# Kernel optimization log

Measured on AMD Instinct MI355X. Metric: run time of the kernel, lower is better.

## Reference

```python
import jax, jax.numpy as jnp
import numpy as np

B, D_IN, H, D_OUT, E = 16384, 512, 1024, 512, 4


def setup_inputs() -> dict:
    key = jax.random.key(0)
    ks = jax.random.split(key, 8)
    x = jax.random.normal(ks[0], (B, D_IN), dtype=jnp.float32)
    command = jax.random.randint(ks[1], (B,), 0, E, dtype=jnp.int64)
    # Per-branch Encoder params: Linear(D_IN->H), Linear(H->H), Linear(H->D_OUT)
    s = 0.02
    W1 = jax.random.normal(ks[2], (E, D_IN, H), dtype=jnp.float32) * s
    b1 = jnp.zeros((E, H), dtype=jnp.float32)
    W2 = jax.random.normal(ks[3], (E, H, H), dtype=jnp.float32) * s
    b2 = jnp.zeros((E, H), dtype=jnp.float32)
    W3 = jax.random.normal(ks[4], (E, H, D_OUT), dtype=jnp.float32) * s
    b3 = jnp.zeros((E, D_OUT), dtype=jnp.float32)
    return {"x": x, "command": command, "W1": W1, "b1": b1,
            "W2": W2, "b2": b2, "W3": W3, "b3": b3}


def reference(x, command, W1, b1, W2, b2, W3, b3):
    # Evaluate all branches as batched GEMMs, then select per-sample branch.
    # Mathematically identical to per-sample dispatch in the torch module.
    h = jax.nn.relu(jnp.einsum('bi,eih->beh', x, W1) + b1)        # [B,E,H]
    h = jax.nn.relu(jnp.einsum('beh,ehk->bek', h, W2) + b2)       # [B,E,H]
    y = jnp.tanh(jnp.einsum('bek,eko->beo', h, W3) + b3)          # [B,E,D_OUT]
    # select branch output per sample according to command
    idx = command.astype(jnp.int32)[:, None, None]                # [B,1,1]
    out = jnp.take_along_axis(y, idx, axis=1)[:, 0, :]            # [B,D_OUT]
    return out
```

## Files before the change

kernel.cpp:

```cpp
#include <hip/hip_runtime.h>


#define B_N   16384
#define DIN   512
#define HID   1024
#define DOUT  512
#define MAXTILES 136

typedef __attribute__((ext_vector_type(8))) short bf16x8;
typedef __attribute__((ext_vector_type(4))) float f32x4;
typedef __attribute__((address_space(3))) unsigned int lds_u32;
typedef const __attribute__((address_space(1))) unsigned int glb_u32;

__device__ __forceinline__ void gll16(const void* g, void* l) {
    __builtin_amdgcn_global_load_lds((glb_u32*)g, (lds_u32*)l, 16, 0, 0);
}

__device__ __forceinline__ unsigned short f2bf(float f) {
    unsigned int u = __float_as_uint(f);
    u += 0x7FFFu + ((u >> 16) & 1u);
    return (unsigned short)(u >> 16);
}

__device__ __forceinline__ float fast_tanh(float x) {
    x = fminf(fmaxf(x, -9.0f), 9.0f);
    float t = __builtin_amdgcn_exp2f(x * 2.8853900817779268f);
    return (t - 1.0f) * __builtin_amdgcn_rcpf(t + 1.0f);
}

__global__ void plan_all_k(const int* __restrict__ cmd, int* __restrict__ ctrl,
                           int* __restrict__ tileExpert, int* __restrict__ tileBase) {
    __shared__ int h[4];
    int tid = threadIdx.x;
    if (tid < 4) h[tid] = 0;
    __syncthreads();
    int c0 = 0, c1 = 0, c2 = 0, c3 = 0;
    for (int i = tid; i < B_N; i += 256) {
        int e = cmd[i] & 3;
        c0 += (e == 0); c1 += (e == 1); c2 += (e == 2); c3 += (e == 3);
    }
    atomicAdd(&h[0], c0); atomicAdd(&h[1], c1);
    atomicAdd(&h[2], c2); atomicAdd(&h[3], c3);
    __syncthreads();
    if (tid == 0) {
        int P = 0, nt = 0;
        for (int e = 0; e < 4; ++e) {
            ctrl[e] = h[e];
            ctrl[4 + e] = 0;
            ctrl[8 + e] = P;
            int tiles = (h[e] + 127) >> 7;
            for (int t = 0; t < tiles; ++t) {
                tileExpert[nt] = e;
                tileBase[nt] = P + t * 128;
                ++nt;
            }
            P += tiles * 128;
        }
        ctrl[12] = P;
        ctrl[13] = nt;
    }
}

__global__ void scatter_k(const int* __restrict__ cmd, int* __restrict__ ctrl,
                          int* __restrict__ perm) {
    int i = blockIdx.x * 256 + threadIdx.x;
    int e = cmd[i] & 3;
    int lane = threadIdx.x & 63;
#pragma unroll
    for (int ee = 0; ee < 4; ++ee) {
        unsigned long long mask = __ballot(e == ee);
        if (e == ee) {
            int leader = __ffsll((unsigned long long)mask) - 1;
            int rank = __popcll(mask & ((1ull << lane) - 1ull));
            int wbase = 0;
            if (lane == leader)
                wbase = atomicAdd(&ctrl[4 + ee], __popcll(mask));
            wbase = __builtin_amdgcn_readfirstlane(wbase);
            perm[ctrl[8 + ee] + wbase + rank] = i;
        }
    }
}

__global__ __launch_bounds__(256) void prep_data_k(
    const float* __restrict__ W1, const float* __restrict__ W2,
    const float* __restrict__ W3, unsigned short* __restrict__ Wt1,
    unsigned short* __restrict__ Wt2, unsigned short* __restrict__ Wt3,
    const float* __restrict__ x, unsigned short* __restrict__ xp,
    int* __restrict__ perm, const int* __restrict__ ctrl)
{
    int b = blockIdx.x;
    if (b < 8192) {
        int e = b >> 11, r = b & 2047;
        const float* W; unsigned short* Wt; int KD, ND, kt, nt;
        if (r < 512)       { W = W1; Wt = Wt1; KD = 512;  ND = 1024; kt = r & 15;           nt = r >> 4; }
        else if (r < 1536) { W = W2; Wt = Wt2; KD = 1024; ND = 1024; kt = (r - 512) & 31;   nt = (r - 512) >> 5; }
        else               { W = W3; Wt = Wt3; KD = 1024; ND = 512;  kt = (r - 1536) & 31;  nt = (r - 1536) >> 5; }
        __shared__ float t[32][33];
        size_t base = (size_t)e * KD * ND;
        int k0 = kt * 32, n0 = nt * 32;
        int tx = threadIdx.x & 31, ty = threadIdx.x >> 5;
#pragma unroll
        for (int s = 0; s < 4; ++s)
            t[ty + s * 8][tx] = W[base + (size_t)(k0 + ty + s * 8) * ND + n0 + tx];
        __syncthreads();
#pragma unroll
        for (int s = 0; s < 4; ++s)
            Wt[base + (size_t)(n0 + ty + s * 8) * KD + k0 + tx] = f2bf(t[tx][ty + s * 8]);
    } else {
        int g = b - 8192;
        int p = g * 4 + (int)(threadIdx.x >> 6);
        if (p >= ctrl[12]) return;
        int lane = threadIdx.x & 63;
        int e = (p >= ctrl[9]) + (p >= ctrl[10]) + (p >= ctrl[11]);
        int segBase = ctrl[8 + e];
        int src;
        if (p < segBase + ctrl[e]) {
            src = perm[p];
        } else {
            src = perm[segBase];
            if (lane == 0) perm[p] = src;
        }
        const float* xr = x + (size_t)src * DIN + lane * 8;
        float4 a = *(const float4*)xr;
        float4 c = *(const float4*)(xr + 4);
        uint4 o;
        o.x = (unsigned)f2bf(a.x) | ((unsigned)f2bf(a.y) << 16);
        o.y = (unsigned)f2bf(a.z) | ((unsigned)f2bf(a.w) << 16);
        o.z = (unsigned)f2bf(c.x) | ((unsigned)f2bf(c.y) << 16);
        o.w = (unsigned)f2bf(c.z) | ((unsigned)f2bf(c.w) << 16);
        *(uint4*)(xp + (size_t)p * DIN + lane * 8) = o;
    }
}

template<int K, int N, int ACT, bool SCATTER_OUT>
__global__ __launch_bounds__(256) void gemm_k(
    const unsigned short* __restrict__ A, const unsigned short* __restrict__ Bt,
    const float* __restrict__ bias, void* __restrict__ Outp,
    const int* __restrict__ ctrl, const int* __restrict__ tileExpert,
    const int* __restrict__ tileBase, const int* __restrict__ perm)
{
    if ((int)blockIdx.x >= ctrl[13]) return;
    const int e = tileExpert[blockIdx.x];
    const int rowBase = tileBase[blockIdx.x];
    const int n0 = blockIdx.y * 128;

    __shared__ unsigned short Als[128 * 64];
    __shared__ unsigned short Bls[128 * 64];

    const int tid = threadIdx.x;
    const int lane = tid & 63;
    const int w = tid >> 6;
    const int wm = w >> 1, wn = w & 1;
    const int lr = lane & 15, lh = lane >> 4;

    f32x4 acc[4][4] = {};

    const int tr = tid >> 3;
    const int tc = tid & 7;
    const int cs = (tc ^ (tr & 7)) * 8;
    const unsigned short* As = A + (size_t)(rowBase + tr) * K + cs;
    const unsigned short* Bs = Bt + ((size_t)e * N + n0 + tr) * K + cs;
    const int ldst = tr * 64 + tc * 8;

    constexpr int NK = K / 64;
    for (int kq = 0; kq < NK; ++kq) {
        const int k0 = kq * 64;
        __syncthreads();
#pragma unroll
        for (int j = 0; j < 4; ++j) {
            gll16(As + (size_t)(j * 32) * K + k0, &Als[j * 2048 + ldst]);
            gll16(Bs + (size_t)(j * 32) * K + k0, &Bls[j * 2048 + ldst]);
        }
        __syncthreads();
#pragma unroll
        for (int kk = 0; kk < 2; ++kk) {
            const int ksl = ((kk * 4 + lh) ^ (lr & 7)) * 8;
            bf16x8 afr[4], bfr[4];
#pragma unroll
            for (int mi = 0; mi < 4; ++mi)
                afr[mi] = *(const bf16x8*)&Als[(wm * 64 + mi * 16 + lr) * 64 + ksl];
#pragma unroll
            for (int ni = 0; ni < 4; ++ni)
                bfr[ni] = *(const bf16x8*)&Bls[(wn * 64 + ni * 16 + lr) * 64 + ksl];
#pragma unroll
            for (int mi = 0; mi < 4; ++mi)
#pragma unroll
                for (int ni = 0; ni < 4; ++ni)
                    acc[mi][ni] = __builtin_amdgcn_mfma_f32_16x16x32_bf16(
                        afr[mi], bfr[ni], acc[mi][ni], 0, 0, 0);
        }
    }

    float bv[4];
    int colv[4];
#pragma unroll
    for (int ni = 0; ni < 4; ++ni) {
        colv[ni] = n0 + wn * 64 + ni * 16 + lr;
        bv[ni] = bias[e * N + colv[ni]];
    }
#pragma unroll
    for (int mi = 0; mi < 4; ++mi) {
#pragma unroll
        for (int r = 0; r < 4; ++r) {
            int rowL = wm * 64 + mi * 16 + lh * 4 + r;
            int gRow = rowBase + rowL;
            int orow = SCATTER_OUT ? perm[gRow] : gRow;
#pragma unroll
            for (int ni = 0; ni < 4; ++ni) {
                float v = acc[mi][ni][r] + bv[ni];
                if (ACT == 0) v = fmaxf(v, 0.0f);
                else          v = fast_tanh(v);
                if (SCATTER_OUT)
                    ((float*)Outp)[(size_t)orow * N + colv[ni]] = v;
                else
                    ((unsigned short*)Outp)[(size_t)orow * N + colv[ni]] = f2bf(v);
            }
        }
    }
}

extern "C" void kernel_launch(void* const* d_in, const int* in_sizes, int n_in,
                              void* d_out, int out_size, void* d_ws, size_t ws_size,
                              hipStream_t stream) {
    const float* x  = (const float*)d_in[0];
    const int*   cmd= (const int*)d_in[1];
    const float* W1 = (const float*)d_in[2];
    const float* b1 = (const float*)d_in[3];
    const float* W2 = (const float*)d_in[4];
    const float* b2 = (const float*)d_in[5];
    const float* W3 = (const float*)d_in[6];
    const float* b3 = (const float*)d_in[7];
    float* out = (float*)d_out;

    char* w = (char*)d_ws;
    int* ctrl       = (int*)w;
    int* tileExpert = ctrl + 64;
    int* tileBase   = ctrl + 224;
    int* perm       = ctrl + 512;
    unsigned short* Wt1 = (unsigned short*)(w + 131072);
    unsigned short* Wt2 = (unsigned short*)(w + 131072 + 4194304);
    unsigned short* Wt3 = (unsigned short*)(w + 131072 + 12582912);
    unsigned short* h1  = (unsigned short*)(w + 131072 + 16777216);
    unsigned short* h2  = h1 + (size_t)16896 * HID;
    unsigned short* xp  = h2;

    plan_all_k<<<1, 256, 0, stream>>>(cmd, ctrl, tileExpert, tileBase);
    scatter_k<<<B_N / 256, 256, 0, stream>>>(cmd, ctrl, perm);
    prep_data_k<<<8192 + 4224, 256, 0, stream>>>(W1, W2, W3, Wt1, Wt2, Wt3,
                                                 x, xp, perm, ctrl);

    gemm_k<DIN, HID, 0, false><<<dim3(MAXTILES, 8), 256, 0, stream>>>(
        xp, Wt1, b1, h1, ctrl, tileExpert, tileBase, perm);
    gemm_k<HID, HID, 0, false><<<dim3(MAXTILES, 8), 256, 0, stream>>>(
        h1, Wt2, b2, h2, ctrl, tileExpert, tileBase, perm);
    gemm_k<HID, DOUT, 1, true><<<dim3(MAXTILES, 4), 256, 0, stream>>>(
        h2, Wt3, b3, out, ctrl, tileExpert, tileBase, perm);
}
```

Measured before the change: 167.9 us.

## Overlap W2/W3 transpose-convert with first GEMM via extra blocks

The prep kernel now transposes and converts only W1 plus the gathered x. The W2 and W3 fp32-to-bf16 transposes move into extra blocks appended to the first GEMM's grid, so they run alongside the layer-1 matrix work instead of before it. This hides the weight conversion bandwidth behind compute. In exchange the GEMM launch has a much larger grid and the shared memory is reused as transpose scratch.

```diff
diff --git a/kernel.cpp b/kernel.cpp
--- a/kernel.cpp
+++ b/kernel.cpp
@@ -81,33 +81,28 @@
     }
 }
 
-__global__ __launch_bounds__(256) void prep_data_k(
-    const float* __restrict__ W1, const float* __restrict__ W2,
-    const float* __restrict__ W3, unsigned short* __restrict__ Wt1,
-    unsigned short* __restrict__ Wt2, unsigned short* __restrict__ Wt3,
+__global__ __launch_bounds__(256) void prep1_k(
+    const float* __restrict__ W1, unsigned short* __restrict__ Wt1,
     const float* __restrict__ x, unsigned short* __restrict__ xp,
     int* __restrict__ perm, const int* __restrict__ ctrl)
 {
     int b = blockIdx.x;
-    if (b < 8192) {
-        int e = b >> 11, r = b & 2047;
-        const float* W; unsigned short* Wt; int KD, ND, kt, nt;
-        if (r < 512)       { W = W1; Wt = Wt1; KD = 512;  ND = 1024; kt = r & 15;           nt = r >> 4; }
-        else if (r < 1536) { W = W2; Wt = Wt2; KD = 1024; ND = 1024; kt = (r - 512) & 31;   nt = (r - 512) >> 5; }
-        else               { W = W3; Wt = Wt3; KD = 1024; ND = 512;  kt = (r - 1536) & 31;  nt = (r - 1536) >> 5; }
+    if (b < 2048) {
+        int e = b >> 9, r = b & 511;
+        int kt = r & 15, nt = r >> 4;
         __shared__ float t[32][33];
-        size_t base = (size_t)e * KD * ND;
+        size_t base = (size_t)e * DIN * HID;
         int k0 = kt * 32, n0 = nt * 32;
         int tx = threadIdx.x & 31, ty = threadIdx.x >> 5;
 #pragma unroll
         for (int s = 0; s < 4; ++s)
-            t[ty + s * 8][tx] = W[base + (size_t)(k0 + ty + s * 8) * ND + n0 + tx];
-        __syncthreads();
-#pragma unroll
-        for (int s = 0; s < 4; ++s)
-            Wt[base + (size_t)(n0 + ty + s * 8) * KD + k0 + tx] = f2bf(t[tx][ty + s * 8]);
+            t[ty + s * 8][tx] = W1[base + (size_t)(k0 + ty + s * 8) * HID + n0 + tx];
+        __syncthreads();
+#pragma unroll
+        for (int s = 0; s < 4; ++s)
+            Wt1[base + (size_t)(n0 + ty + s * 8) * DIN + k0 + tx] = f2bf(t[tx][ty + s * 8]);
     } else {
-        int g = b - 8192;
+        int g = b - 2048;
         int p = g * 4 + (int)(threadIdx.x >> 6);
         if (p >= ctrl[12]) return;
         int lane = threadIdx.x & 63;
@@ -132,20 +127,43 @@
     }
 }
 
-template<int K, int N, int ACT, bool SCATTER_OUT>
+template<int K, int N, int ACT, bool SCATTER_OUT, bool FUSE_TW>
 __global__ __launch_bounds__(256) void gemm_k(
     const unsigned short* __restrict__ A, const unsigned short* __restrict__ Bt,
     const float* __restrict__ bias, void* __restrict__ Outp,
     const int* __restrict__ ctrl, const int* __restrict__ tileExpert,
-    const int* __restrict__ tileBase, const int* __restrict__ perm)
+    const int* __restrict__ tileBase, const int* __restrict__ perm,
+    const float* __restrict__ W2, const float* __restrict__ W3,
+    unsigned short* __restrict__ Wt2, unsigned short* __restrict__ Wt3)
 {
+    __shared__ unsigned short Als[128 * 64];
+    __shared__ unsigned short Bls[128 * 64];
+
+    if (FUSE_TW && (int)blockIdx.x >= MAXTILES) {
+        int T = ((int)blockIdx.x - MAXTILES) + 768 * (int)blockIdx.y;
+        const float* W; unsigned short* Wt; int KD, ND, kt, nt, e;
+        if (T < 4096) { W = W2; Wt = Wt2; KD = HID; ND = HID;
+                        e = T >> 10; int r = T & 1023; kt = r & 31; nt = r >> 5; }
+        else { int T2 = T - 4096; W = W3; Wt = Wt3; KD = HID; ND = DOUT;
+               e = T2 >> 9; int r = T2 & 511; kt = r & 31; nt = r >> 5; }
+        float (*t)[33] = (float(*)[33])Als;
+        size_t base = (size_t)e * KD * ND;
+        int k0 = kt * 32, n0 = nt * 32;
+        int tx = threadIdx.x & 31, ty = threadIdx.x >> 5;
+#pragma unroll
+        for (int s = 0; s < 4; ++s)
+            t[ty + s * 8][tx] = W[base + (size_t)(k0 + ty + s * 8) * ND + n0 + tx];
+        __syncthreads();
+#pragma unroll
+        for (int s = 0; s < 4; ++s)
+            Wt[base + (size_t)(n0 + ty + s * 8) * KD + k0 + tx] = f2bf(t[tx][ty + s * 8]);
+        return;
+    }
+
     if ((int)blockIdx.x >= ctrl[13]) return;
     const int e = tileExpert[blockIdx.x];
     const int rowBase = tileBase[blockIdx.x];
     const int n0 = blockIdx.y * 128;
-
-    __shared__ unsigned short Als[128 * 64];
-    __shared__ unsigned short Bls[128 * 64];
 
     const int tid = threadIdx.x;
     const int lane = tid & 63;
@@ -246,13 +264,14 @@
 
     plan_all_k<<<1, 256, 0, stream>>>(cmd, ctrl, tileExpert, tileBase);
     scatter_k<<<B_N / 256, 256, 0, stream>>>(cmd, ctrl, perm);
-    prep_data_k<<<8192 + 4224, 256, 0, stream>>>(W1, W2, W3, Wt1, Wt2, Wt3,
-                                                 x, xp, perm, ctrl);
-
-    gemm_k<DIN, HID, 0, false><<<dim3(MAXTILES, 8), 256, 0, stream>>>(
-        xp, Wt1, b1, h1, ctrl, tileExpert, tileBase, perm);
-    gemm_k<HID, HID, 0, false><<<dim3(MAXTILES, 8), 256, 0, stream>>>(
-        h1, Wt2, b2, h2, ctrl, tileExpert, tileBase, perm);
-    gemm_k<HID, DOUT, 1, true><<<dim3(MAXTILES, 4), 256, 0, stream>>>(
-        h2, Wt3, b3, out, ctrl, tileExpert, tileBase, perm);
-}
+    prep1_k<<<2048 + 4224, 256, 0, stream>>>(W1, Wt1, x, xp, perm, ctrl);
+
+    gemm_k<DIN, HID, 0, false, true><<<dim3(MAXTILES + 768, 8), 256, 0, stream>>>(
+        xp, Wt1, b1, h1, ctrl, tileExpert, tileBase, perm, W2, W3, Wt2, Wt3);
+    gemm_k<HID, HID, 0, false, false><<<dim3(MAXTILES, 8), 256, 0, stream>>>(
+        h1, Wt2, b2, h2, ctrl, tileExpert, tileBase, perm,
+        nullptr, nullptr, nullptr, nullptr);
+    gemm_k<HID, DOUT, 1, true, false><<<dim3(MAXTILES, 4), 256, 0, stream>>>(
+        h2, Wt3, b3, out, ctrl, tileExpert, tileBase, perm,
+        nullptr, nullptr, nullptr, nullptr);
+}
```

Result: no change. 169.1 us (+0.7%).

## Enlarge grouped GEMM tiles to 256 rows with 512-thread blocks

Applied to the files above, without the earlier changes.

The tile planner now emits 256-row tiles per expert, plus a flagged 128-row tail tile, instead of uniform 128-row tiles. The GEMM kernel runs 512 threads (8 waves) with a 256xBN tile (BN=256 for layers 1-2, 128 for layer 3). This raises arithmetic intensity per LDS load and cuts redundant global traffic. Half tiles wrap their A-row loads and skip out-of-range stores. In exchange there are fewer blocks (68x4) for the CUs, more accumulator registers per wave, and possible occupancy loss.

```diff
diff --git a/kernel.cpp b/kernel.cpp
--- a/kernel.cpp
+++ b/kernel.cpp
@@ -5,7 +5,7 @@
 #define DIN   512
 #define HID   1024
 #define DOUT  512
-#define MAXTILES 136
+#define MAXT256 68
 
 typedef __attribute__((ext_vector_type(8))) short bf16x8;
 typedef __attribute__((ext_vector_type(4))) float f32x4;
@@ -48,13 +48,19 @@
             ctrl[e] = h[e];
             ctrl[4 + e] = 0;
             ctrl[8 + e] = P;
-            int tiles = (h[e] + 127) >> 7;
-            for (int t = 0; t < tiles; ++t) {
+            int cp = ((h[e] + 127) >> 7) << 7;
+            int nfull = cp >> 8;
+            for (int t = 0; t < nfull; ++t) {
                 tileExpert[nt] = e;
-                tileBase[nt] = P + t * 128;
+                tileBase[nt] = P + t * 256;
                 ++nt;
             }
-            P += tiles * 128;
+            if (cp & 128) {
+                tileExpert[nt] = e | 4;
+                tileBase[nt] = P + nfull * 256;
+                ++nt;
+            }
+            P += cp;
         }
         ctrl[12] = P;
         ctrl[13] = nt;
@@ -132,58 +138,69 @@
     }
 }
 
-template<int K, int N, int ACT, bool SCATTER_OUT>
-__global__ __launch_bounds__(256) void gemm_k(
+template<int K, int N, int BN, int ACT, bool SCATTER_OUT>
+__global__ __launch_bounds__(512, 2) void gemm_k(
     const unsigned short* __restrict__ A, const unsigned short* __restrict__ Bt,
     const float* __restrict__ bias, void* __restrict__ Outp,
     const int* __restrict__ ctrl, const int* __restrict__ tileExpert,
     const int* __restrict__ tileBase, const int* __restrict__ perm)
 {
+    constexpr int WN = BN / 64;
+    constexpr int WM = 8 / WN;
+    constexpr int MI = 16 / WM;
+    constexpr int BCALLS = BN / 64;
+
+    __shared__ unsigned short Als[256 * 64];
+    __shared__ unsigned short Bls[BN * 64];
+
     if ((int)blockIdx.x >= ctrl[13]) return;
-    const int e = tileExpert[blockIdx.x];
+    const int te = tileExpert[blockIdx.x];
+    const int e = te & 3;
+    const int TM = (te & 4) ? 128 : 256;
+    const int wrapMask = TM - 1;
     const int rowBase = tileBase[blockIdx.x];
-    const int n0 = blockIdx.y * 128;
-
-    __shared__ unsigned short Als[128 * 64];
-    __shared__ unsigned short Bls[128 * 64];
+    const int n0 = blockIdx.y * BN;
 
     const int tid = threadIdx.x;
     const int lane = tid & 63;
     const int w = tid >> 6;
-    const int wm = w >> 1, wn = w & 1;
+    const int wm = w / WN, wn = w % WN;
     const int lr = lane & 15, lh = lane >> 4;
 
-    f32x4 acc[4][4] = {};
+    f32x4 acc[MI][4] = {};
 
     const int tr = tid >> 3;
     const int tc = tid & 7;
     const int cs = (tc ^ (tr & 7)) * 8;
-    const unsigned short* As = A + (size_t)(rowBase + tr) * K + cs;
-    const unsigned short* Bs = Bt + ((size_t)e * N + n0 + tr) * K + cs;
-    const int ldst = tr * 64 + tc * 8;
-
-    constexpr int NK = K / 64;
-    for (int kq = 0; kq < NK; ++kq) {
+    const int ldst = tid * 8;
+    int arow[4];
+#pragma unroll
+    for (int j = 0; j < 4; ++j)
+        arow[j] = rowBase + ((tr + j * 64) & wrapMask);
+
+    for (int kq = 0; kq < K / 64; ++kq) {
         const int k0 = kq * 64;
         __syncthreads();
 #pragma unroll
-        for (int j = 0; j < 4; ++j) {
-            gll16(As + (size_t)(j * 32) * K + k0, &Als[j * 2048 + ldst]);
-            gll16(Bs + (size_t)(j * 32) * K + k0, &Bls[j * 2048 + ldst]);
-        }
+        for (int j = 0; j < 4; ++j)
+            gll16(A + (size_t)arow[j] * K + cs + k0, &Als[j * 4096 + ldst]);
+#pragma unroll
+        for (int j = 0; j < BCALLS; ++j)
+            gll16(Bt + ((size_t)e * N + n0 + tr + j * 64) * K + cs + k0,
+                  &Bls[j * 4096 + ldst]);
         __syncthreads();
 #pragma unroll
         for (int kk = 0; kk < 2; ++kk) {
             const int ksl = ((kk * 4 + lh) ^ (lr & 7)) * 8;
-            bf16x8 afr[4], bfr[4];
-#pragma unroll
-            for (int mi = 0; mi < 4; ++mi)
-                afr[mi] = *(const bf16x8*)&Als[(wm * 64 + mi * 16 + lr) * 64 + ksl];
+            bf16x8 afr[MI], bfr[4];
+#pragma unroll
+            for (int mi = 0; mi < MI; ++mi)
+                afr[mi] = *(const bf16x8*)&Als[(wm * (MI * 16) + mi * 16 + lr) * 64 + ksl];
 #pragma unroll
             for (int ni = 0; ni < 4; ++ni)
                 bfr[ni] = *(const bf16x8*)&Bls[(wn * 64 + ni * 16 + lr) * 64 + ksl];
 #pragma unroll
-            for (int mi = 0; mi < 4; ++mi)
+            for (int mi = 0; mi < MI; ++mi)
 #pragma unroll
                 for (int ni = 0; ni < 4; ++ni)
                     acc[mi][ni] = __builtin_amdgcn_mfma_f32_16x16x32_bf16(
@@ -199,10 +216,11 @@
         bv[ni] = bias[e * N + colv[ni]];
     }
 #pragma unroll
-    for (int mi = 0; mi < 4; ++mi) {
+    for (int mi = 0; mi < MI; ++mi) {
 #pragma unroll
         for (int r = 0; r < 4; ++r) {
-            int rowL = wm * 64 + mi * 16 + lh * 4 + r;
+            int rowL = wm * (MI * 16) + mi * 16 + lh * 4 + r;
+            if (rowL >= TM) continue;
             int gRow = rowBase + rowL;
             int orow = SCATTER_OUT ? perm[gRow] : gRow;
 #pragma unroll
@@ -249,10 +267,10 @@
     prep_data_k<<<8192 + 4224, 256, 0, stream>>>(W1, W2, W3, Wt1, Wt2, Wt3,
                                                  x, xp, perm, ctrl);
 
-    gemm_k<DIN, HID, 0, false><<<dim3(MAXTILES, 8), 256, 0, stream>>>(
+    gemm_k<DIN, HID, 256, 0, false><<<dim3(MAXT256, 4), 512, 0, stream>>>(
         xp, Wt1, b1, h1, ctrl, tileExpert, tileBase, perm);
-    gemm_k<HID, HID, 0, false><<<dim3(MAXTILES, 8), 256, 0, stream>>>(
+    gemm_k<HID, HID, 256, 0, false><<<dim3(MAXT256, 4), 512, 0, stream>>>(
         h1, Wt2, b2, h2, ctrl, tileExpert, tileBase, perm);
-    gemm_k<HID, DOUT, 1, true><<<dim3(MAXTILES, 4), 256, 0, stream>>>(
+    gemm_k<HID, DOUT, 128, 1, true><<<dim3(MAXT256, 4), 512, 0, stream>>>(
         h2, Wt3, b3, out, ctrl, tileExpert, tileBase, perm);
 }
```

Result: slower. 212.3 us (+26.4%).

## Use 256x256 double-buffered 8-wave GEMM tiles for the first two layers

Applied to the files above, without the earlier changes.

Adds a gemm8_k kernel with 512 threads computing 256x256 output tiles. It double-buffers 128 KB of LDS and interleaves global_load_lds staging of the next K-slice with MFMA quarter-phases under raised wave priority. The planner now emits both 256-row tiles (a half tile is flagged when an expert's padded count is odd in 128s) and 128-row tiles, so the final tanh layer keeps the old 128x128 kernel. The goal is more operand reuse per LDS byte and overlap of loads with compute in layers 1 and 2. In exchange, the bigger tiles give fewer blocks and lower occupancy, and the half tiles waste MFMA work through wrapped rows.

```diff
diff --git a/kernel.cpp b/kernel.cpp
--- a/kernel.cpp
+++ b/kernel.cpp
@@ -5,7 +5,8 @@
 #define DIN   512
 #define HID   1024
 #define DOUT  512
-#define MAXTILES 136
+#define MAXT256 68
+#define MAXT128 136
 
 typedef __attribute__((ext_vector_type(8))) short bf16x8;
 typedef __attribute__((ext_vector_type(4))) float f32x4;
@@ -29,7 +30,8 @@
 }
 
 __global__ void plan_all_k(const int* __restrict__ cmd, int* __restrict__ ctrl,
-                           int* __restrict__ tileExpert, int* __restrict__ tileBase) {
+                           int* __restrict__ t256E, int* __restrict__ t256B,
+                           int* __restrict__ t128E, int* __restrict__ t128B) {
     __shared__ int h[4];
     int tid = threadIdx.x;
     if (tid < 4) h[tid] = 0;
@@ -43,21 +45,28 @@
     atomicAdd(&h[2], c2); atomicAdd(&h[3], c3);
     __syncthreads();
     if (tid == 0) {
-        int P = 0, nt = 0;
+        int P = 0, n256 = 0, n128 = 0;
         for (int e = 0; e < 4; ++e) {
             ctrl[e] = h[e];
             ctrl[4 + e] = 0;
             ctrl[8 + e] = P;
-            int tiles = (h[e] + 127) >> 7;
-            for (int t = 0; t < tiles; ++t) {
-                tileExpert[nt] = e;
-                tileBase[nt] = P + t * 128;
-                ++nt;
+            int cp = ((h[e] + 127) >> 7) << 7;
+            int nfull = cp >> 8;
+            for (int t = 0; t < nfull; ++t) {
+                t256E[n256] = e; t256B[n256] = P + t * 256; ++n256;
             }
-            P += tiles * 128;
+            if (cp & 128) {
+                t256E[n256] = e | 4; t256B[n256] = P + nfull * 256; ++n256;
+            }
+            int nt = cp >> 7;
+            for (int t = 0; t < nt; ++t) {
+                t128E[n128] = e; t128B[n128] = P + t * 128; ++n128;
+            }
+            P += cp;
         }
         ctrl[12] = P;
-        ctrl[13] = nt;
+        ctrl[13] = n256;
+        ctrl[14] = n128;
     }
 }
 
@@ -132,16 +141,128 @@
     }
 }
 
-template<int K, int N, int ACT, bool SCATTER_OUT>
-__global__ __launch_bounds__(256) void gemm_k(
+#define VMW(n) asm volatile("s_waitcnt vmcnt(" #n ")" ::: "memory")
+#define BAR  do { asm volatile("" ::: "memory"); __builtin_amdgcn_s_barrier(); \
+                  asm volatile("" ::: "memory"); } while (0)
+
+template<int K, int N>
+__global__ __launch_bounds__(512, 2) void gemm8_k(
     const unsigned short* __restrict__ A, const unsigned short* __restrict__ Bt,
-    const float* __restrict__ bias, void* __restrict__ Outp,
-    const int* __restrict__ ctrl, const int* __restrict__ tileExpert,
-    const int* __restrict__ tileBase, const int* __restrict__ perm)
+    const float* __restrict__ bias, unsigned short* __restrict__ Outp,
+    const int* __restrict__ ctrl, const int* __restrict__ t256E,
+    const int* __restrict__ t256B)
 {
+    __shared__ unsigned short LDS[65536];
     if ((int)blockIdx.x >= ctrl[13]) return;
-    const int e = tileExpert[blockIdx.x];
-    const int rowBase = tileBase[blockIdx.x];
+    const int te = t256E[blockIdx.x];
+    const int e = te & 3;
+    const int TM = (te & 4) ? 128 : 256;
+    const int wrapMask = TM - 1;
+    const int rowBase = t256B[blockIdx.x];
+    const int n0 = blockIdx.y * 256;
+
+    const int tid = threadIdx.x;
+    const int lane = tid & 63;
+    const int w = tid >> 6;
+    const int wm = w >> 2, wn = w & 3;
+    const int lr = lane & 15, lh = lane >> 4;
+
+    f32x4 acc[2][2][4][2] = {};
+
+    const int tr = tid >> 3, tc = tid & 7;
+    const int cs = (tc ^ (tr & 7)) * 8;
+    size_t aoff[2][2], boff[2][2];
+#pragma unroll
+    for (int h = 0; h < 2; ++h)
+#pragma unroll
+        for (int j = 0; j < 2; ++j) {
+            aoff[h][j] = (size_t)(rowBase + ((h * 128 + j * 64 + tr) & wrapMask)) * K + cs;
+            boff[h][j] = ((size_t)e * N + n0 + h * 128 + j * 64 + tr) * K + cs;
+        }
+    const int ksl0 = (lh ^ (lr & 7)) * 8;
+    const int ksl1 = ((4 + lh) ^ (lr & 7)) * 8;
+
+#define STAGE_A(tt, h) do { const int _tb = (tt) & 1, _k = (tt) * 64;          \
+        gll16(A + aoff[h][0] + _k, &LDS[_tb * 32768 + (h) * 8192 + tid * 8]);  \
+        gll16(A + aoff[h][1] + _k, &LDS[_tb * 32768 + (h) * 8192 + 4096 + tid * 8]); } while (0)
+#define STAGE_B(tt, h) do { const int _tb = (tt) & 1, _k = (tt) * 64;          \
+        gll16(Bt + boff[h][0] + _k, &LDS[_tb * 32768 + 16384 + (h) * 8192 + tid * 8]); \
+        gll16(Bt + boff[h][1] + _k, &LDS[_tb * 32768 + 16384 + (h) * 8192 + 4096 + tid * 8]); } while (0)
+#define QPHASE(tb, MH, NH) do {                                                \
+        bf16x8 afr[4][2], bfr[2][2];                                           \
+        _Pragma("unroll") for (int mi = 0; mi < 4; ++mi) {                     \
+            int arow = (MH) * 128 + wm * 64 + mi * 16 + lr;                    \
+            afr[mi][0] = *(const bf16x8*)&LDS[(tb) * 32768 + arow * 64 + ksl0];\
+            afr[mi][1] = *(const bf16x8*)&LDS[(tb) * 32768 + arow * 64 + ksl1];\
+        }                                                                      \
+        _Pragma("unroll") for (int ni = 0; ni < 2; ++ni) {                     \
+            int brow = (NH) * 128 + wn * 32 + ni * 16 + lr;                    \
+            bfr[ni][0] = *(const bf16x8*)&LDS[(tb) * 32768 + 16384 + brow * 64 + ksl0]; \
+            bfr[ni][1] = *(const bf16x8*)&LDS[(tb) * 32768 + 16384 + brow * 64 + ksl1]; \
+        }                                                                      \
+        __builtin_amdgcn_s_setprio(1);                                         \
+        _Pragma("unroll") for (int mi = 0; mi < 4; ++mi)                       \
+        _Pragma("unroll") for (int ni = 0; ni < 2; ++ni) {                     \
+            acc[MH][NH][mi][ni] = __builtin_amdgcn_mfma_f32_16x16x32_bf16(     \
+                afr[mi][0], bfr[ni][0], acc[MH][NH][mi][ni], 0, 0, 0);         \
+            acc[MH][NH][mi][ni] = __builtin_amdgcn_mfma_f32_16x16x32_bf16(     \
+                afr[mi][1], bfr[ni][1], acc[MH][NH][mi][ni], 0, 0, 0);         \
+        }                                                                      \
+        __builtin_amdgcn_s_setprio(0); } while (0)
+
+    constexpr int NT = K / 64;
+    STAGE_A(0, 0); STAGE_B(0, 0); STAGE_A(0, 1); STAGE_B(0, 1);
+    for (int t = 0; t < NT - 1; ++t) {
+        const int tb = t & 1;
+        STAGE_A(t + 1, 0); VMW(6); BAR; QPHASE(tb, 0, 0);
+        STAGE_B(t + 1, 0); VMW(6); BAR; QPHASE(tb, 1, 0);
+        STAGE_A(t + 1, 1); VMW(6); BAR; QPHASE(tb, 0, 1);
+        STAGE_B(t + 1, 1);         BAR; QPHASE(tb, 1, 1);
+    }
+    {
+        const int tb = (NT - 1) & 1;
+        VMW(4); BAR; QPHASE(tb, 0, 0);
+        VMW(2); BAR; QPHASE(tb, 1, 0);
+        VMW(0); BAR; QPHASE(tb, 0, 1);
+                BAR; QPHASE(tb, 1, 1);
+    }
+#undef STAGE_A
+#undef STAGE_B
+#undef QPHASE
+
+#pragma unroll
+    for (int mh = 0; mh < 2; ++mh) {
+        if (!(TM == 128 && mh == 1)) {
+#pragma unroll
+            for (int nh = 0; nh < 2; ++nh)
+#pragma unroll
+                for (int ni = 0; ni < 2; ++ni) {
+                    int col = n0 + nh * 128 + wn * 32 + ni * 16 + lr;
+                    float bv = bias[e * N + col];
+#pragma unroll
+                    for (int mi = 0; mi < 4; ++mi)
+#pragma unroll
+                        for (int r = 0; r < 4; ++r) {
+                            int rowL = mh * 128 + wm * 64 + mi * 16 + lh * 4 + r;
+                            float v = acc[mh][nh][mi][ni][r] + bv;
+                            v = fmaxf(v, 0.0f);
+                            Outp[(size_t)(rowBase + rowL) * N + col] = f2bf(v);
+                        }
+                }
+        }
+    }
+}
+
+template<int K, int N>
+__global__ __launch_bounds__(256) void gemm128_k(
+    const unsigned short* __restrict__ A, const unsigned short* __restrict__ Bt,
+    const float* __restrict__ bias, float* __restrict__ Outp,
+    const int* __restrict__ ctrl, const int* __restrict__ t128E,
+    const int* __restrict__ t128B, const int* __restrict__ perm)
+{
+    if ((int)blockIdx.x >= ctrl[14]) return;
+    const int e = t128E[blockIdx.x];
+    const int rowBase = t128B[blockIdx.x];
     const int n0 = blockIdx.y * 128;
 
     __shared__ unsigned short Als[128 * 64];
@@ -162,8 +283,7 @@
     const unsigned short* Bs = Bt + ((size_t)e * N + n0 + tr) * K + cs;
     const int ldst = tr * 64 + tc * 8;
 
-    constexpr int NK = K / 64;
-    for (int kq = 0; kq < NK; ++kq) {
+    for (int kq = 0; kq < K / 64; ++kq) {
         const int k0 = kq * 64;
         __syncthreads();
 #pragma unroll
@@ -203,17 +323,11 @@
 #pragma unroll
         for (int r = 0; r < 4; ++r) {
             int rowL = wm * 64 + mi * 16 + lh * 4 + r;
-            int gRow = rowBase + rowL;
-            int orow = SCATTER_OUT ? perm[gRow] : gRow;
+            int orow = perm[rowBase + rowL];
 #pragma unroll
             for (int ni = 0; ni < 4; ++ni) {
-                float v = acc[mi][ni][r] + bv[ni];
-                if (ACT == 0) v = fmaxf(v, 0.0f);
-                else          v = fast_tanh(v);
-                if (SCATTER_OUT)
-                    ((float*)Outp)[(size_t)orow * N + colv[ni]] = v;
-                else
-                    ((unsigned short*)Outp)[(size_t)orow * N + colv[ni]] = f2bf(v);
+                float v = fast_tanh(acc[mi][ni][r] + bv[ni]);
+                Outp[(size_t)orow * N + colv[ni]] = v;
             }
         }
     }
@@ -233,10 +347,12 @@
     float* out = (float*)d_out;
 
     char* w = (char*)d_ws;
-    int* ctrl       = (int*)w;
-    int* tileExpert = ctrl + 64;
-    int* tileBase   = ctrl + 224;
-    int* perm       = ctrl + 512;
+    int* ctrl  = (int*)w;
+    int* t256E = ctrl + 64;
+    int* t256B = ctrl + 160;
+    int* t128E = ctrl + 256;
+    int* t128B = ctrl + 448;
+    int* perm  = ctrl + 768;
     unsigned short* Wt1 = (unsigned short*)(w + 131072);
     unsigned short* Wt2 = (unsigned short*)(w + 131072 + 4194304);
     unsigned short* Wt3 = (unsigned short*)(w + 131072 + 12582912);
@@ -244,15 +360,15 @@
     unsigned short* h2  = h1 + (size_t)16896 * HID;
     unsigned short* xp  = h2;
 
-    plan_all_k<<<1, 256, 0, stream>>>(cmd, ctrl, tileExpert, tileBase);
+    plan_all_k<<<1, 256, 0, stream>>>(cmd, ctrl, t256E, t256B, t128E, t128B);
     scatter_k<<<B_N / 256, 256, 0, stream>>>(cmd, ctrl, perm);
     prep_data_k<<<8192 + 4224, 256, 0, stream>>>(W1, W2, W3, Wt1, Wt2, Wt3,
                                                  x, xp, perm, ctrl);
 
-    gemm_k<DIN, HID, 0, false><<<dim3(MAXTILES, 8), 256, 0, stream>>>(
-        xp, Wt1, b1, h1, ctrl, tileExpert, tileBase, perm);
-    gemm_k<HID, HID, 0, false><<<dim3(MAXTILES, 8), 256, 0, stream>>>(
-        h1, Wt2, b2, h2, ctrl, tileExpert, tileBase, perm);
-    gemm_k<HID, DOUT, 1, true><<<dim3(MAXTILES, 4), 256, 0, stream>>>(
-        h2, Wt3, b3, out, ctrl, tileExpert, tileBase, perm);
-}
+    gemm8_k<DIN, HID><<<dim3(MAXT256, 4), 512, 0, stream>>>(
+        xp, Wt1, b1, h1, ctrl, t256E, t256B);
+    gemm8_k<HID, HID><<<dim3(MAXT256, 4), 512, 0, stream>>>(
+        h1, Wt2, b2, h2, ctrl, t256E, t256B);
+    gemm128_k<HID, DOUT><<<dim3(MAXT128, 4), 256, 0, stream>>>(
+        h2, Wt3, b3, out, ctrl, t128E, t128B, perm);
+}
```

New measurement: 190.6 us. 1.14x slower.
